# Kernel optimization log

Measured on AMD Instinct MI355X. Metric: run time of the kernel, lower is better.

The kernel has to match this reference:

```python
import jax, jax.numpy as jnp
import numpy as np

NL, DM, DI, DS, DC, DTR, NC = 2, 512, 1024, 8, 4, 32, 50
B, CIN, L = 4, 1, 2048


def _layernorm(x, g, b, eps=1e-5):
    mu = jnp.mean(x, axis=-1, keepdims=True)
    var = jnp.mean((x - mu) ** 2, axis=-1, keepdims=True)
    return (x - mu) * jax.lax.rsqrt(var + eps) * g + b


def _selective_scan(u, dt, A, Bm, Cm, D):
    # u, dt: [B,L,DI]; A: [DI,DS]; Bm, Cm: [B,L,DS]; D: [DI]
    dA = jnp.exp(dt[..., None] * A)                       # [B,L,DI,DS]
    dBu = dt[..., None] * Bm[:, :, None, :] * u[..., None]  # [B,L,DI,DS]

    def step(h, inp):
        dA_t, dBu_t, C_t = inp
        h = dA_t * h + dBu_t                              # [B,DI,DS]
        y = jnp.einsum('bdn,bn->bd', h, C_t)
        return h, y

    h0 = jnp.zeros((u.shape[0], A.shape[0], A.shape[1]), u.dtype)
    xs = (dA.transpose(1, 0, 2, 3), dBu.transpose(1, 0, 2, 3), Cm.transpose(1, 0, 2))
    _, ys = jax.lax.scan(step, h0, xs)                    # ys: [L,B,DI]
    return ys.transpose(1, 0, 2) + u * D


def _mamba(x, in_w, conv_w, conv_b, xp_w, dt_w, dt_b, A_log, D, out_w):
    # x: [B,L,DM]
    xz = x @ in_w.T                                       # [B,L,2*DI]
    u, z = jnp.split(xz, 2, axis=-1)
    # depthwise causal conv1d over L
    upad = jnp.pad(u, ((0, 0), (DC - 1, 0), (0, 0)))
    uc = conv_b + sum(upad[:, k:k + u.shape[1], :] * conv_w[:, k] for k in range(DC))
    uc = jax.nn.silu(uc)
    xdbl = uc @ xp_w.T                                    # [B,L,DTR+2*DS]
    dt = xdbl[..., :DTR]
    Bm = xdbl[..., DTR:DTR + DS]
    Cm = xdbl[..., DTR + DS:]
    dt = jax.nn.softplus(dt @ dt_w.T + dt_b)              # [B,L,DI]
    A = -jnp.exp(A_log)
    y = _selective_scan(uc, dt, A, Bm, Cm, D)
    y = y * jax.nn.silu(z)
    return y @ out_w.T                                    # [B,L,DM]


def _forward(x, inp_w, inp_b, norm_g, norm_b, in_w, conv_w, conv_b, xp_w,
             dt_w, dt_b, A_log, Dp, out_w, fnorm_g, fnorm_b, head_w, head_b):
    h = x.transpose(0, 2, 1) @ inp_w.T + inp_b            # [B,L,DM]
    for i in range(NL):
        res = h
        hn = _layernorm(h, norm_g[i], norm_b[i])
        h = res + _mamba(hn, in_w[i], conv_w[i], conv_b[i], xp_w[i],
                         dt_w[i], dt_b[i], A_log[i], Dp[i], out_w[i])
    h = _layernorm(h, fnorm_g, fnorm_b)
    h = jnp.mean(h, axis=1)                               # [B,DM]
    return h @ head_w.T + head_b                          # [B,NC]


def setup_inputs() -> dict:
    key = jax.random.key(0)
    ks = jax.random.split(key, 10)
    f = jnp.float32
    s = 0.02
    x = jax.random.normal(ks[0], (B, CIN, L), f)
    inp_w = jax.random.normal(ks[1], (DM, CIN), f) * s
    inp_b = jnp.zeros((DM,), f)
    norm_g = jnp.ones((NL, DM), f)
    norm_b = jnp.zeros((NL, DM), f)
    in_w = jax.random.normal(ks[2], (NL, 2 * DI, DM), f) * s
    conv_w = jax.random.normal(ks[3], (NL, DI, DC), f) * s
    conv_b = jnp.zeros((NL, DI), f)
    xp_w = jax.random.normal(ks[4], (NL, DTR + 2 * DS, DI), f) * s
    dt_w = jax.random.normal(ks[5], (NL, DI, DTR), f) * s
    dt_b = jax.random.uniform(ks[6], (NL, DI), f, -5.0, -2.0)
    A_log = jnp.log(jnp.broadcast_to(jnp.arange(1, DS + 1, dtype=f), (NL, DI, DS)))
    Dp = jnp.ones((NL, DI), f)
    out_w = jax.random.normal(ks[7], (NL, DM, DI), f) * s
    fnorm_g = jnp.ones((DM,), f)
    fnorm_b = jnp.zeros((DM,), f)
    head_w = jax.random.normal(ks[8], (NC, DM), f) * s
    head_b = jnp.zeros((NC,), f)
    return dict(x=x, inp_w=inp_w, inp_b=inp_b, norm_g=norm_g, norm_b=norm_b,
                in_w=in_w, conv_w=conv_w, conv_b=conv_b, xp_w=xp_w, dt_w=dt_w,
                dt_b=dt_b, A_log=A_log, Dp=Dp, out_w=out_w, fnorm_g=fnorm_g,
                fnorm_b=fnorm_b, head_w=head_w, head_b=head_b)


def reference(x, inp_w, inp_b, norm_g, norm_b, in_w, conv_w, conv_b, xp_w,
              dt_w, dt_b, A_log, Dp, out_w, fnorm_g, fnorm_b, head_w, head_b):
    return _forward(x, inp_w, inp_b, norm_g, norm_b, in_w, conv_w, conv_b, xp_w,
                    dt_w, dt_b, A_log, Dp, out_w, fnorm_g, fnorm_b, head_w, head_b)
```

## Files before the change

### kernel.cpp

```cpp
#include <hip/hip_runtime.h>
#include <hip/hip_bf16.h>
#include <cstddef>

constexpr int NL = 2, DM = 512, DI = 1024, DS = 8, DC = 4, DTR = 32, NC = 50;
constexpr int B = 4, L = 2048;
constexpr int M = B * L;
constexpr int XZW = 2 * DI;
constexpr int XDW = DTR + 2 * DS;
constexpr int NCH = 64, CH = L / NCH;
constexpr int XSK = 8;

typedef __bf16 bf16_t;
typedef bf16_t bf16x8 __attribute__((ext_vector_type(8)));
typedef bf16_t bf16x4 __attribute__((ext_vector_type(4)));
typedef float f32x4 __attribute__((ext_vector_type(4)));

__global__ void embed_k(const float* __restrict__ x, const float* __restrict__ iw,
                        const float* __restrict__ ib, float* __restrict__ h) {
    int idx = blockIdx.x * blockDim.x + threadIdx.x;
    if (idx >= M * DM / 4) return;
    int d4 = idx % (DM / 4);
    int m = idx / (DM / 4);
    float4 w = reinterpret_cast<const float4*>(iw)[d4];
    float4 bb = reinterpret_cast<const float4*>(ib)[d4];
    float xv = x[m];
    float4 r;
    r.x = xv * w.x + bb.x; r.y = xv * w.y + bb.y;
    r.z = xv * w.z + bb.z; r.w = xv * w.w + bb.w;
    reinterpret_cast<float4*>(h)[idx] = r;
}

constexpr int WN1 = NL * XZW * DM / 4;
constexpr int WN2 = NL * XDW * DI / 4;
constexpr int WN3 = NL * DI * DTR / 4;
constexpr int WN4 = NL * DM * DI / 4;
constexpr int WNT = WN1 + WN2 + WN3 + WN4;
__global__ void cvt_ws_k(const float* __restrict__ s1, const float* __restrict__ s2,
                         const float* __restrict__ s3, const float* __restrict__ s4,
                         bf16_t* __restrict__ d1, bf16_t* __restrict__ d2,
                         bf16_t* __restrict__ d3, bf16_t* __restrict__ d4) {
    int i4 = blockIdx.x * 256 + threadIdx.x;
    const float* s; bf16_t* d; int off;
    if (i4 < WN1) { s = s1; d = d1; off = i4; }
    else if (i4 < WN1 + WN2) { s = s2; d = d2; off = i4 - WN1; }
    else if (i4 < WN1 + WN2 + WN3) { s = s3; d = d3; off = i4 - WN1 - WN2; }
    else if (i4 < WNT) { s = s4; d = d4; off = i4 - WN1 - WN2 - WN3; }
    else return;
    float4 f = reinterpret_cast<const float4*>(s)[off];
    bf16x4 v;
    v[0] = (bf16_t)f.x; v[1] = (bf16_t)f.y; v[2] = (bf16_t)f.z; v[3] = (bf16_t)f.w;
    *reinterpret_cast<bf16x4*>(d + (size_t)off * 4) = v;
}

__global__ __launch_bounds__(256) void layernorm_k(const float* __restrict__ in,
                                                   const float* __restrict__ g,
                                                   const float* __restrict__ b,
                                                   bf16_t* __restrict__ out) {
    int row = blockIdx.x;
    const float* x = in + (size_t)row * DM;
    int t = threadIdx.x;
    float v0 = x[t], v1 = x[t + 256];
    float s = v0 + v1, sq = v0 * v0 + v1 * v1;
    for (int o = 32; o > 0; o >>= 1) {
        s += __shfl_down(s, o);
        sq += __shfl_down(sq, o);
    }
    __shared__ float sums[8];
    if ((t & 63) == 0) { sums[t >> 6] = s; sums[4 + (t >> 6)] = sq; }
    __syncthreads();
    float tot = sums[0] + sums[1] + sums[2] + sums[3];
    float totq = sums[4] + sums[5] + sums[6] + sums[7];
    float mu = tot * (1.0f / DM);
    float var = totq * (1.0f / DM) - mu * mu;
    float rs = rsqrtf(var + 1e-5f);
    out[(size_t)row * DM + t]       = (bf16_t)((v0 - mu) * rs * g[t] + b[t]);
    out[(size_t)row * DM + t + 256] = (bf16_t)((v1 - mu) * rs * g[t + 256] + b[t + 256]);
}

template <int BM, int BN, int EPI, typename TC, int SK>
__global__ __launch_bounds__(256) void gemm_mfma(const bf16_t* __restrict__ A, int lda,
                                                 const bf16_t* __restrict__ W, int ldw,
                                                 const float* __restrict__ bias,
                                                 TC* __restrict__ C, int ldc,
                                                 int Nr, int K) {
    constexpr int WM = BM / 2, WN = BN / 2;
    constexpr int FM = WM / 16, FN = WN / 16;
    constexpr int ACH = BM * 32 / (256 * 8);
    constexpr int WCH = BN * 32 / (256 * 8);
    __shared__ bf16_t As[2][BM * 32];
    __shared__ bf16_t Ws[2][BN * 32];

    int tid = threadIdx.x;
    int m0 = blockIdx.y * BM, n0 = blockIdx.x * BN;
    int Ktot = K;
    if constexpr (SK > 1) {
        int s = blockIdx.z;
        Ktot = K / SK;
        A += (size_t)s * Ktot;
        W += (size_t)s * Ktot;
        C += (size_t)s * (size_t)(gridDim.y * BM) * ldc;
    }
    int wave = tid >> 6, lane = tid & 63;
    int wr = wave >> 1, wc = wave & 1;
    int lr = lane & 15, lk = lane >> 4;

    auto load_tile = [&](int k0, bf16x8* ra, bf16x8* rw) {
#pragma unroll
        for (int c = 0; c < ACH; ++c) {
            int e = tid + c * 256;
            int r = e >> 2, g = e & 3;
            ra[c] = *reinterpret_cast<const bf16x8*>(A + (size_t)(m0 + r) * lda + k0 + g * 8);
        }
#pragma unroll
        for (int c = 0; c < WCH; ++c) {
            int e = tid + c * 256;
            int r = e >> 2, g = e & 3;
            bf16x8 z;
#pragma unroll
            for (int q = 0; q < 8; q++) z[q] = (bf16_t)0.0f;
            rw[c] = (n0 + r < Nr)
                ? *reinterpret_cast<const bf16x8*>(W + (size_t)(n0 + r) * ldw + k0 + g * 8)
                : z;
        }
    };
    auto store_tile = [&](const bf16x8* ra, const bf16x8* rw, int buf) {
#pragma unroll
        for (int c = 0; c < ACH; ++c) {
            int e = tid + c * 256;
            int r = e >> 2, g = e & 3;
            int slot = g ^ ((r >> 1) & 3);
            *reinterpret_cast<bf16x8*>(&As[buf][r * 32 + slot * 8]) = ra[c];
        }
#pragma unroll
        for (int c = 0; c < WCH; ++c) {
            int e = tid + c * 256;
            int r = e >> 2, g = e & 3;
            int slot = g ^ ((r >> 1) & 3);
            *reinterpret_cast<bf16x8*>(&Ws[buf][r * 32 + slot * 8]) = rw[c];
        }
    };

    f32x4 acc[FM][FN];
#pragma unroll
    for (int i = 0; i < FM; i++)
#pragma unroll
        for (int j = 0; j < FN; j++)
#pragma unroll
            for (int q = 0; q < 4; q++) acc[i][j][q] = 0.0f;

    bf16x8 pa[ACH], pw[WCH];
    load_tile(0, pa, pw);
    store_tile(pa, pw, 0);
    __syncthreads();

    int nt = Ktot / 32;
    int cur = 0;
    for (int t = 0; t < nt; ++t) {
        bool pf = (t + 1 < nt);
        if (pf) load_tile((t + 1) * 32, pa, pw);

        bf16x8 af[FM], bfr[FN];
#pragma unroll
        for (int mi = 0; mi < FM; mi++) {
            int r = wr * WM + mi * 16 + lr;
            int slot = lk ^ ((r >> 1) & 3);
            af[mi] = *reinterpret_cast<const bf16x8*>(&As[cur][r * 32 + slot * 8]);
        }
#pragma unroll
        for (int ni = 0; ni < FN; ni++) {
            int r = wc * WN + ni * 16 + lr;
            int slot = lk ^ ((r >> 1) & 3);
            bfr[ni] = *reinterpret_cast<const bf16x8*>(&Ws[cur][r * 32 + slot * 8]);
        }
#pragma unroll
        for (int mi = 0; mi < FM; mi++)
#pragma unroll
            for (int ni = 0; ni < FN; ni++)
                acc[mi][ni] = __builtin_amdgcn_mfma_f32_16x16x32_bf16(af[mi], bfr[ni], acc[mi][ni], 0, 0, 0);

        if (pf) {
            store_tile(pa, pw, cur ^ 1);
            __syncthreads();
            cur ^= 1;
        }
    }

#pragma unroll
    for (int mi = 0; mi < FM; mi++) {
#pragma unroll
        for (int ni = 0; ni < FN; ni++) {
            int col = n0 + wc * WN + ni * 16 + lr;
            if (col >= Nr) continue;
#pragma unroll
            for (int i = 0; i < 4; i++) {
                int row = m0 + wr * WM + mi * 16 + lk * 4 + i;
                size_t idx = (size_t)row * ldc + col;
                float v = acc[mi][ni][i];
                if constexpr (EPI == 0) {
                    C[idx] = (TC)v;
                } else if constexpr (EPI == 1) {
                    C[idx] += v;
                } else {
                    float s = v + bias[col];
                    C[idx] = (TC)((s > 20.0f) ? s : __logf(1.0f + __expf(s)));
                }
            }
        }
    }
}

__global__ void xproj_reduce_k(const float* __restrict__ part, float* __restrict__ xdbl,
                               bf16_t* __restrict__ xdt) {
    int idx = blockIdx.x * blockDim.x + threadIdx.x;
    if (idx >= M * XDW) return;
    int m = idx / XDW, j = idx % XDW;
    float s = 0.f;
#pragma unroll
    for (int sp = 0; sp < XSK; sp++) s += part[((size_t)sp * M + m) * 64 + j];
    xdbl[idx] = s;
    if (j < DTR) xdt[(size_t)m * DTR + j] = (bf16_t)s;
}

__global__ void conv_silu_k(const bf16_t* __restrict__ xz, const float* __restrict__ cw,
                            const float* __restrict__ cb, bf16_t* __restrict__ uc) {
    int idx = blockIdx.x * blockDim.x + threadIdx.x;
    if (idx >= M * DI) return;
    int d = idx % DI;
    int m = idx / DI;
    int b = m / L, l = m % L;
    float acc = cb[d];
#pragma unroll
    for (int k = 0; k < DC; k++) {
        int ls = l + k - (DC - 1);
        if (ls >= 0) acc += (float)xz[(size_t)(b * L + ls) * XZW + d] * cw[d * DC + k];
    }
    uc[idx] = (bf16_t)(acc / (1.0f + __expf(-acc)));
}

__global__ __launch_bounds__(256) void scan_part_k(const bf16_t* __restrict__ dt,
                                                   const bf16_t* __restrict__ uc,
                                                   const float* __restrict__ xdbl,
                                                   const float* __restrict__ A_log,
                                                   float* __restrict__ hpart,
                                                   float* __restrict__ aprod) {
    int gid = blockIdx.x * 256 + threadIdx.x;
    if (gid >= B * NCH * DI) return;
    int d = gid % DI;
    int c = (gid / DI) % NCH;
    int b = gid / (DI * NCH);
    float Av[DS];
#pragma unroll
    for (int n = 0; n < DS; n++) Av[n] = -__expf(A_log[d * DS + n]);
    float h[DS] = {};
    float ap[DS];
#pragma unroll
    for (int n = 0; n < DS; n++) ap[n] = 1.0f;
    int l0 = c * CH;
    for (int t = 0; t < CH; t++) {
        size_t row = (size_t)b * L + l0 + t;
        float dtv = (float)dt[row * DI + d];
        float uv = (float)uc[row * DI + d];
        const float* xr = xdbl + row * XDW;
        float du = dtv * uv;
#pragma unroll
        for (int n = 0; n < DS; n++) {
            float dA = __expf(dtv * Av[n]);
            h[n] = dA * h[n] + du * xr[DTR + n];
            ap[n] *= dA;
        }
    }
    size_t base = (((size_t)b * DI + d) * NCH + c) * DS;
#pragma unroll
    for (int n = 0; n < DS; n++) {
        hpart[base + n] = h[n];
        aprod[base + n] = ap[n];
    }
}

__global__ void scan_combine_k(float* __restrict__ hpart, const float* __restrict__ aprod) {
    int gid = blockIdx.x * blockDim.x + threadIdx.x;
    if (gid >= B * DI * DS) return;
    int n = gid & (DS - 1);
    int d = (gid >> 3) & (DI - 1);
    int b = gid >> 13;
    size_t base = ((size_t)(b * DI + d) * NCH) * DS + n;
    float hrun = 0.f;
    for (int c = 0; c < NCH; c++) {
        size_t idx = base + (size_t)c * DS;
        float ap = aprod[idx];
        float hp = hpart[idx];
        hpart[idx] = hrun;
        hrun = ap * hrun + hp;
    }
}

__global__ __launch_bounds__(256) void scan_emit_k(const bf16_t* __restrict__ dt,
                                                   const bf16_t* __restrict__ uc,
                                                   const float* __restrict__ xdbl,
                                                   const bf16_t* __restrict__ xz,
                                                   const float* __restrict__ A_log,
                                                   const float* __restrict__ Dp,
                                                   const float* __restrict__ hpart,
                                                   bf16_t* __restrict__ y) {
    int gid = blockIdx.x * 256 + threadIdx.x;
    if (gid >= B * NCH * DI) return;
    int d = gid % DI;
    int c = (gid / DI) % NCH;
    int b = gid / (DI * NCH);
    float Av[DS];
#pragma unroll
    for (int n = 0; n < DS; n++) Av[n] = -__expf(A_log[d * DS + n]);
    float h[DS];
    size_t sbase = (((size_t)b * DI + d) * NCH + c) * DS;
#pragma unroll
    for (int n = 0; n < DS; n++) h[n] = hpart[sbase + n];
    float Dv = Dp[d];
    int l0 = c * CH;
    for (int t = 0; t < CH; t++) {
        size_t row = (size_t)b * L + l0 + t;
        float dtv = (float)dt[row * DI + d];
        float uv = (float)uc[row * DI + d];
        const float* xr = xdbl + row * XDW;
        float du = dtv * uv;
        float yv = 0.f;
#pragma unroll
        for (int n = 0; n < DS; n++) {
            float dA = __expf(dtv * Av[n]);
            h[n] = dA * h[n] + du * xr[DTR + n];
            yv += h[n] * xr[DTR + DS + n];
        }
        yv += uv * Dv;
        float zv = (float)xz[row * XZW + DI + d];
        yv *= zv / (1.0f + __expf(-zv));
        y[row * DI + d] = (bf16_t)yv;
    }
}

__global__ __launch_bounds__(256) void mean_part_k(const bf16_t* __restrict__ hn,
                                                   float* __restrict__ partial) {
    int c = blockIdx.x;
    int b = blockIdx.y;
    int t = threadIdx.x;
    float s0 = 0.f, s1 = 0.f;
    for (int l = 0; l < L / 32; l++) {
        const bf16_t* row = hn + (size_t)(b * L + c * (L / 32) + l) * DM;
        s0 += (float)row[t];
        s1 += (float)row[t + 256];
    }
    partial[(size_t)(b * 32 + c) * DM + t] = s0;
    partial[(size_t)(b * 32 + c) * DM + t + 256] = s1;
}

__global__ void mean_fin_k(const float* __restrict__ partial, float* __restrict__ hmean) {
    int idx = blockIdx.x * blockDim.x + threadIdx.x;
    if (idx >= B * DM) return;
    int b = idx / DM, d = idx % DM;
    float s = 0.f;
#pragma unroll
    for (int c = 0; c < 32; c++) s += partial[(size_t)(b * 32 + c) * DM + d];
    hmean[idx] = s * (1.0f / L);
}

__global__ void head_k(const float* __restrict__ hmean, const float* __restrict__ hw,
                       const float* __restrict__ hb, float* __restrict__ out) {
    int t = threadIdx.x;
    if (t >= B * NC) return;
    int b = t / NC, c = t % NC;
    float acc = hb[c];
    for (int k = 0; k < DM; k++) acc += hmean[b * DM + k] * hw[c * DM + k];
    out[t] = acc;
}

extern "C" void kernel_launch(void* const* d_in, const int* in_sizes, int n_in,
                              void* d_out, int out_size, void* d_ws, size_t ws_size,
                              hipStream_t stream) {
    const float* x      = (const float*)d_in[0];
    const float* inp_w  = (const float*)d_in[1];
    const float* inp_b  = (const float*)d_in[2];
    const float* norm_g = (const float*)d_in[3];
    const float* norm_b = (const float*)d_in[4];
    const float* in_w   = (const float*)d_in[5];
    const float* conv_w = (const float*)d_in[6];
    const float* conv_b = (const float*)d_in[7];
    const float* xp_w   = (const float*)d_in[8];
    const float* dt_w   = (const float*)d_in[9];
    const float* dt_b   = (const float*)d_in[10];
    const float* A_log  = (const float*)d_in[11];
    const float* Dp     = (const float*)d_in[12];
    const float* out_w  = (const float*)d_in[13];
    const float* fnorm_g = (const float*)d_in[14];
    const float* fnorm_b = (const float*)d_in[15];
    const float* head_w = (const float*)d_in[16];
    const float* head_b = (const float*)d_in[17];
    float* out = (float*)d_out;

    char* p = (char*)d_ws;
    float*  h     = (float*)p;  p += (size_t)M * DM * 4;
    bf16_t* hn    = (bf16_t*)p; p += (size_t)M * DM * 2;
    bf16_t* xz    = (bf16_t*)p; p += (size_t)M * XZW * 2;
    bf16_t* uc    = (bf16_t*)p; p += (size_t)M * DI * 2;
    float*  xdbl  = (float*)p;  p += (size_t)M * XDW * 4;
    bf16_t* xdt   = (bf16_t*)p; p += (size_t)M * DTR * 2;
    bf16_t* dtb   = (bf16_t*)p; p += (size_t)M * DI * 2;
    bf16_t* yb    = (bf16_t*)p; p += (size_t)M * DI * 2;
    float*  hpart = (float*)p;  p += (size_t)B * DI * NCH * DS * 4;
    float*  aprod = (float*)p;  p += (size_t)B * DI * NCH * DS * 4;
    float*  xpart = (float*)p;  p += (size_t)XSK * M * 64 * 4;
    float*  partial = (float*)p; p += (size_t)B * 32 * DM * 4;
    float*  hmean = (float*)p;  p += (size_t)B * DM * 4;
    bf16_t* wb_in = (bf16_t*)p; p += (size_t)NL * XZW * DM * 2;
    bf16_t* wb_xp = (bf16_t*)p; p += (size_t)NL * XDW * DI * 2;
    bf16_t* wb_dt = (bf16_t*)p; p += (size_t)NL * DI * DTR * 2;
    bf16_t* wb_out = (bf16_t*)p; p += (size_t)NL * DM * DI * 2;

    cvt_ws_k<<<(WNT + 255) / 256, 256, 0, stream>>>(in_w, xp_w, dt_w, out_w,
                                                    wb_in, wb_xp, wb_dt, wb_out);
    embed_k<<<(M * DM / 4 + 255) / 256, 256, 0, stream>>>(x, inp_w, inp_b, h);

    for (int i = 0; i < NL; i++) {
        const bf16_t* inw_i = wb_in + (size_t)i * XZW * DM;
        const float* cw_i  = conv_w + (size_t)i * DI * DC;
        const float* cb_i  = conv_b + (size_t)i * DI;
        const bf16_t* xpw_i = wb_xp + (size_t)i * XDW * DI;
        const bf16_t* dtw_i = wb_dt + (size_t)i * DI * DTR;
        const float* dtb_i = dt_b + (size_t)i * DI;
        const float* Al_i  = A_log + (size_t)i * DI * DS;
        const float* Dp_i  = Dp + (size_t)i * DI;
        const bf16_t* ow_i  = wb_out + (size_t)i * DM * DI;

        layernorm_k<<<M, 256, 0, stream>>>(h, norm_g + i * DM, norm_b + i * DM, hn);
        gemm_mfma<128, 64, 0, bf16_t, 1><<<dim3(XZW / 64, M / 128), 256, 0, stream>>>(
            hn, DM, inw_i, DM, nullptr, xz, XZW, XZW, DM);
        conv_silu_k<<<(M * DI + 255) / 256, 256, 0, stream>>>(xz, cw_i, cb_i, uc);
        gemm_mfma<64, 64, 0, float, XSK><<<dim3(1, M / 64, XSK), 256, 0, stream>>>(
            uc, DI, xpw_i, DI, nullptr, xpart, 64, XDW, DI);
        xproj_reduce_k<<<(M * XDW + 255) / 256, 256, 0, stream>>>(xpart, xdbl, xdt);
        gemm_mfma<64, 64, 2, bf16_t, 1><<<dim3(DI / 64, M / 64), 256, 0, stream>>>(
            xdt, DTR, dtw_i, DTR, dtb_i, dtb, DI, DI, DTR);
        scan_part_k<<<(B * NCH * DI) / 256, 256, 0, stream>>>(dtb, uc, xdbl, Al_i, hpart, aprod);
        scan_combine_k<<<(B * DI * DS + 255) / 256, 256, 0, stream>>>(hpart, aprod);
        scan_emit_k<<<(B * NCH * DI) / 256, 256, 0, stream>>>(dtb, uc, xdbl, xz, Al_i, Dp_i, hpart, yb);
        gemm_mfma<64, 64, 1, float, 1><<<dim3(DM / 64, M / 64), 256, 0, stream>>>(
            yb, DI, ow_i, DI, nullptr, h, DM, DM, DI);
    }

    layernorm_k<<<M, 256, 0, stream>>>(h, fnorm_g, fnorm_b, hn);
    mean_part_k<<<dim3(32, B), 256, 0, stream>>>(hn, partial);
    mean_fin_k<<<(B * DM + 255) / 256, 256, 0, stream>>>(partial, hmean);
    head_k<<<1, 256, 0, stream>>>(hmean, head_w, head_b, out);
}
```

Baseline: 539.3 us.

## Vectorize conv, scan state layout, and mean reduction memory accesses

Conv+SiLU now processes 8 channels per thread with 16-byte bf16 loads and stores plus float4 weight loads. The scan kernels load B/C and A_log as float4. The hpart/aprod layout changes to [b,chunk,d,n] so the combine kernel reads contiguously across threads and part/emit use vector stores and loads. The mean reduction uses bf16x8 loads with 4 row-subgroups, producing 128 partials per batch. The aim is fewer memory instructions and better coalescing, though the scan part/emit per-thread 32-byte accesses are now strided by d*DS.

```diff
diff --git a/kernel.cpp b/kernel.cpp
--- a/kernel.cpp
+++ b/kernel.cpp
@@ -221,20 +221,48 @@
     if (j < DTR) xdt[(size_t)m * DTR + j] = (bf16_t)s;
 }
 
-__global__ void conv_silu_k(const bf16_t* __restrict__ xz, const float* __restrict__ cw,
-                            const float* __restrict__ cb, bf16_t* __restrict__ uc) {
+__global__ __launch_bounds__(256) void conv_silu_k(const bf16_t* __restrict__ xz,
+                                                   const float* __restrict__ cw,
+                                                   const float* __restrict__ cb,
+                                                   bf16_t* __restrict__ uc) {
     int idx = blockIdx.x * blockDim.x + threadIdx.x;
-    if (idx >= M * DI) return;
-    int d = idx % DI;
-    int m = idx / DI;
+    if (idx >= M * DI / 8) return;
+    int d8 = idx % (DI / 8);
+    int m = idx / (DI / 8);
     int b = m / L, l = m % L;
-    float acc = cb[d];
+    int d0 = d8 * 8;
+
+    float acc[8];
+    {
+        float4 c0 = *reinterpret_cast<const float4*>(cb + d0);
+        float4 c1 = *reinterpret_cast<const float4*>(cb + d0 + 4);
+        acc[0] = c0.x; acc[1] = c0.y; acc[2] = c0.z; acc[3] = c0.w;
+        acc[4] = c1.x; acc[5] = c1.y; acc[6] = c1.z; acc[7] = c1.w;
+    }
+    float4 w[8];
+#pragma unroll
+    for (int j = 0; j < 8; j++)
+        w[j] = *reinterpret_cast<const float4*>(cw + (size_t)(d0 + j) * DC);
+
 #pragma unroll
     for (int k = 0; k < DC; k++) {
         int ls = l + k - (DC - 1);
-        if (ls >= 0) acc += (float)xz[(size_t)(b * L + ls) * XZW + d] * cw[d * DC + k];
-    }
-    uc[idx] = (bf16_t)(acc / (1.0f + __expf(-acc)));
+        if (ls < 0) continue;
+        bf16x8 v = *reinterpret_cast<const bf16x8*>(xz + (size_t)(b * L + ls) * XZW + d0);
+        float wk[8] = {w[0].x, w[1].x, w[2].x, w[3].x, w[4].x, w[5].x, w[6].x, w[7].x};
+        if (k == 1) { wk[0]=w[0].y; wk[1]=w[1].y; wk[2]=w[2].y; wk[3]=w[3].y; wk[4]=w[4].y; wk[5]=w[5].y; wk[6]=w[6].y; wk[7]=w[7].y; }
+        if (k == 2) { wk[0]=w[0].z; wk[1]=w[1].z; wk[2]=w[2].z; wk[3]=w[3].z; wk[4]=w[4].z; wk[5]=w[5].z; wk[6]=w[6].z; wk[7]=w[7].z; }
+        if (k == 3) { wk[0]=w[0].w; wk[1]=w[1].w; wk[2]=w[2].w; wk[3]=w[3].w; wk[4]=w[4].w; wk[5]=w[5].w; wk[6]=w[6].w; wk[7]=w[7].w; }
+#pragma unroll
+        for (int j = 0; j < 8; j++) acc[j] += (float)v[j] * wk[j];
+    }
+    bf16x8 o;
+#pragma unroll
+    for (int j = 0; j < 8; j++) {
+        float a = acc[j];
+        o[j] = (bf16_t)(a / (1.0f + __expf(-a)));
+    }
+    *reinterpret_cast<bf16x8*>(uc + (size_t)m * DI + d0) = o;
 }
 
 __global__ __launch_bounds__(256) void scan_part_k(const bf16_t* __restrict__ dt,
@@ -249,8 +277,12 @@
     int c = (gid / DI) % NCH;
     int b = gid / (DI * NCH);
     float Av[DS];
-#pragma unroll
-    for (int n = 0; n < DS; n++) Av[n] = -__expf(A_log[d * DS + n]);
+    {
+        float4 a0 = *reinterpret_cast<const float4*>(A_log + d * DS);
+        float4 a1 = *reinterpret_cast<const float4*>(A_log + d * DS + 4);
+        Av[0] = -__expf(a0.x); Av[1] = -__expf(a0.y); Av[2] = -__expf(a0.z); Av[3] = -__expf(a0.w);
+        Av[4] = -__expf(a1.x); Av[5] = -__expf(a1.y); Av[6] = -__expf(a1.z); Av[7] = -__expf(a1.w);
+    }
     float h[DS] = {};
     float ap[DS];
 #pragma unroll
@@ -260,33 +292,35 @@
         size_t row = (size_t)b * L + l0 + t;
         float dtv = (float)dt[row * DI + d];
         float uv = (float)uc[row * DI + d];
-        const float* xr = xdbl + row * XDW;
+        const float4* xr4 = reinterpret_cast<const float4*>(xdbl + row * XDW + DTR);
+        float4 b0 = xr4[0], b1 = xr4[1];
+        float Bv[DS] = {b0.x, b0.y, b0.z, b0.w, b1.x, b1.y, b1.z, b1.w};
         float du = dtv * uv;
 #pragma unroll
         for (int n = 0; n < DS; n++) {
             float dA = __expf(dtv * Av[n]);
-            h[n] = dA * h[n] + du * xr[DTR + n];
+            h[n] = dA * h[n] + du * Bv[n];
             ap[n] *= dA;
         }
     }
-    size_t base = (((size_t)b * DI + d) * NCH + c) * DS;
-#pragma unroll
-    for (int n = 0; n < DS; n++) {
-        hpart[base + n] = h[n];
-        aprod[base + n] = ap[n];
-    }
+    size_t base = (((size_t)(b * NCH + c) * DI) + d) * DS;
+    f32x4* hp4 = reinterpret_cast<f32x4*>(hpart + base);
+    f32x4* ap4 = reinterpret_cast<f32x4*>(aprod + base);
+    f32x4 v0, v1, w0, w1;
+#pragma unroll
+    for (int n = 0; n < 4; n++) { v0[n] = h[n]; v1[n] = h[n + 4]; w0[n] = ap[n]; w1[n] = ap[n + 4]; }
+    hp4[0] = v0; hp4[1] = v1;
+    ap4[0] = w0; ap4[1] = w1;
 }
 
 __global__ void scan_combine_k(float* __restrict__ hpart, const float* __restrict__ aprod) {
     int gid = blockIdx.x * blockDim.x + threadIdx.x;
     if (gid >= B * DI * DS) return;
-    int n = gid & (DS - 1);
-    int d = (gid >> 3) & (DI - 1);
+    int dn = gid & (DI * DS - 1);
     int b = gid >> 13;
-    size_t base = ((size_t)(b * DI + d) * NCH) * DS + n;
     float hrun = 0.f;
     for (int c = 0; c < NCH; c++) {
-        size_t idx = base + (size_t)c * DS;
+        size_t idx = ((size_t)(b * NCH + c) * DI * DS) + dn;
         float ap = aprod[idx];
         float hp = hpart[idx];
         hpart[idx] = hrun;
@@ -308,26 +342,37 @@
     int c = (gid / DI) % NCH;
     int b = gid / (DI * NCH);
     float Av[DS];
-#pragma unroll
-    for (int n = 0; n < DS; n++) Av[n] = -__expf(A_log[d * DS + n]);
+    {
+        float4 a0 = *reinterpret_cast<const float4*>(A_log + d * DS);
+        float4 a1 = *reinterpret_cast<const float4*>(A_log + d * DS + 4);
+        Av[0] = -__expf(a0.x); Av[1] = -__expf(a0.y); Av[2] = -__expf(a0.z); Av[3] = -__expf(a0.w);
+        Av[4] = -__expf(a1.x); Av[5] = -__expf(a1.y); Av[6] = -__expf(a1.z); Av[7] = -__expf(a1.w);
+    }
     float h[DS];
-    size_t sbase = (((size_t)b * DI + d) * NCH + c) * DS;
-#pragma unroll
-    for (int n = 0; n < DS; n++) h[n] = hpart[sbase + n];
+    {
+        size_t base = (((size_t)(b * NCH + c) * DI) + d) * DS;
+        const f32x4* hp4 = reinterpret_cast<const f32x4*>(hpart + base);
+        f32x4 v0 = hp4[0], v1 = hp4[1];
+#pragma unroll
+        for (int n = 0; n < 4; n++) { h[n] = v0[n]; h[n + 4] = v1[n]; }
+    }
     float Dv = Dp[d];
     int l0 = c * CH;
     for (int t = 0; t < CH; t++) {
         size_t row = (size_t)b * L + l0 + t;
         float dtv = (float)dt[row * DI + d];
         float uv = (float)uc[row * DI + d];
-        const float* xr = xdbl + row * XDW;
+        const float4* xr4 = reinterpret_cast<const float4*>(xdbl + row * XDW + DTR);
+        float4 b0 = xr4[0], b1 = xr4[1], c0 = xr4[2], c1 = xr4[3];
+        float Bv[DS] = {b0.x, b0.y, b0.z, b0.w, b1.x, b1.y, b1.z, b1.w};
+        float Cv[DS] = {c0.x, c0.y, c0.z, c0.w, c1.x, c1.y, c1.z, c1.w};
         float du = dtv * uv;
         float yv = 0.f;
 #pragma unroll
         for (int n = 0; n < DS; n++) {
             float dA = __expf(dtv * Av[n]);
-            h[n] = dA * h[n] + du * xr[DTR + n];
-            yv += h[n] * xr[DTR + DS + n];
+            h[n] = dA * h[n] + du * Bv[n];
+            yv += h[n] * Cv[n];
         }
         yv += uv * Dv;
         float zv = (float)xz[row * XZW + DI + d];
@@ -341,14 +386,20 @@
     int c = blockIdx.x;
     int b = blockIdx.y;
     int t = threadIdx.x;
-    float s0 = 0.f, s1 = 0.f;
-    for (int l = 0; l < L / 32; l++) {
-        const bf16_t* row = hn + (size_t)(b * L + c * (L / 32) + l) * DM;
-        s0 += (float)row[t];
-        s1 += (float)row[t + 256];
-    }
-    partial[(size_t)(b * 32 + c) * DM + t] = s0;
-    partial[(size_t)(b * 32 + c) * DM + t + 256] = s1;
+    int d0 = (t & 63) * 8;
+    int rsub = t >> 6;
+    float s[8] = {};
+    for (int l = rsub; l < 64; l += 4) {
+        bf16x8 v = *reinterpret_cast<const bf16x8*>(hn + (size_t)(b * L + c * 64 + l) * DM + d0);
+#pragma unroll
+        for (int j = 0; j < 8; j++) s[j] += (float)v[j];
+    }
+    float* dst = partial + ((size_t)(b * 32 + c) * 4 + rsub) * DM + d0;
+    f32x4 o0, o1;
+#pragma unroll
+    for (int j = 0; j < 4; j++) { o0[j] = s[j]; o1[j] = s[j + 4]; }
+    reinterpret_cast<f32x4*>(dst)[0] = o0;
+    reinterpret_cast<f32x4*>(dst)[1] = o1;
 }
 
 __global__ void mean_fin_k(const float* __restrict__ partial, float* __restrict__ hmean) {
@@ -356,8 +407,7 @@
     if (idx >= B * DM) return;
     int b = idx / DM, d = idx % DM;
     float s = 0.f;
-#pragma unroll
-    for (int c = 0; c < 32; c++) s += partial[(size_t)(b * 32 + c) * DM + d];
+    for (int c = 0; c < 128; c++) s += partial[((size_t)b * 128 + c) * DM + d];
     hmean[idx] = s * (1.0f / L);
 }
 
@@ -406,7 +456,7 @@
     float*  hpart = (float*)p;  p += (size_t)B * DI * NCH * DS * 4;
     float*  aprod = (float*)p;  p += (size_t)B * DI * NCH * DS * 4;
     float*  xpart = (float*)p;  p += (size_t)XSK * M * 64 * 4;
-    float*  partial = (float*)p; p += (size_t)B * 32 * DM * 4;
+    float*  partial = (float*)p; p += (size_t)B * 128 * DM * 4;
     float*  hmean = (float*)p;  p += (size_t)B * DM * 4;
     bf16_t* wb_in = (bf16_t*)p; p += (size_t)NL * XZW * DM * 2;
     bf16_t* wb_xp = (bf16_t*)p; p += (size_t)NL * XDW * DI * 2;
@@ -431,7 +481,7 @@
         layernorm_k<<<M, 256, 0, stream>>>(h, norm_g + i * DM, norm_b + i * DM, hn);
         gemm_mfma<128, 64, 0, bf16_t, 1><<<dim3(XZW / 64, M / 128), 256, 0, stream>>>(
             hn, DM, inw_i, DM, nullptr, xz, XZW, XZW, DM);
-        conv_silu_k<<<(M * DI + 255) / 256, 256, 0, stream>>>(xz, cw_i, cb_i, uc);
+        conv_silu_k<<<(M * DI / 8 + 255) / 256, 256, 0, stream>>>(xz, cw_i, cb_i, uc);
         gemm_mfma<64, 64, 0, float, XSK><<<dim3(1, M / 64, XSK), 256, 0, stream>>>(
             uc, DI, xpw_i, DI, nullptr, xpart, 64, XDW, DI);
         xproj_reduce_k<<<(M * XDW + 255) / 256, 256, 0, stream>>>(xpart, xdbl, xdt);
```

Result: faster. 497.7 us (-7.7%).
